# Kernel tuning notes

Hardware: AMD Instinct MI355X
Metric: run time of the kernel (lower is better)

Reference implementation:

```python
import jax, jax.numpy as jnp
import numpy as np

B, N, DIM, HID = 32, 10000, 64, 128


def _linear_params(key, fan_in, fan_out):
    kw, kb = jax.random.split(key)
    bound = 1.0 / np.sqrt(fan_in)
    w = jax.random.uniform(kw, (fan_out, fan_in), jnp.float32, -bound, bound)
    b = jax.random.uniform(kb, (fan_out,), jnp.float32, -bound, bound)
    return w, b


def setup_inputs() -> dict:
    key = jax.random.key(0)
    ks = jax.random.split(key, 7)
    x = jax.random.normal(ks[0], (B, N, DIM), jnp.float32)
    adj_col = jax.random.uniform(ks[1], (N,), jnp.float32)
    n2e_w, n2e_b = _linear_params(ks[2], 2 * DIM, HID)
    e2e_w, e2e_b = _linear_params(ks[3], HID, HID)
    e2n_w, e2n_b = _linear_params(ks[4], HID, HID)
    n2n_w, n2n_b = _linear_params(ks[5], HID, HID)
    out_w, out_b = _linear_params(ks[6], DIM + HID, DIM)
    return {
        "x": x, "adj_col": adj_col,
        "n2e_w": n2e_w, "n2e_b": n2e_b,
        "e2e_w": e2e_w, "e2e_b": e2e_b,
        "e2n_w": e2n_w, "e2n_b": e2n_b,
        "n2n_w": n2n_w, "n2n_b": n2n_b,
        "out_w": out_w, "out_b": out_b,
        "i": 5, "num": 4, "node_size": 2000,
    }


def reference(x, adj_col, n2e_w, n2e_b, e2e_w, e2e_b, e2n_w, e2n_b,
              n2n_w, n2n_b, out_w, out_b, i, num, node_size):
    # The torch loop over (num+1) chunks is an execution tiling; mathematically it
    # computes a full sum over all N nodes. We vectorize it in one pass.
    starter = x[:, i, :]                                   # [B, dim]
    ender = jnp.broadcast_to(starter[:, None, :], x.shape)  # [B, N, dim]
    c = jnp.concatenate([x, ender], axis=-1)               # [B, N, 2*dim]
    h = jax.nn.relu(jnp.einsum('bnd,hd->bnh', c, n2e_w) + n2e_b)
    h = jax.nn.relu(jnp.einsum('bnh,gh->bng', h, e2e_w) + e2e_b)
    h = h * adj_col[None, :, None]                         # adjacency mask
    s = jnp.sum(h, axis=1)                                 # [B, hid]
    y = jax.nn.relu(s @ e2n_w.T + e2n_b)
    y = jax.nn.relu(y @ n2n_w.T + n2n_b)
    out = jnp.concatenate([starter, y], axis=-1) @ out_w.T + out_b  # [B, dim]
    return out
```

## Files before the change

### kernel.cpp

```cpp
#include <hip/hip_runtime.h>
#include <hip/hip_bf16.h>

typedef float f32x4 __attribute__((ext_vector_type(4)));
typedef short bf16x8 __attribute__((ext_vector_type(8)));
typedef unsigned short u16;
typedef unsigned int u32;

#define NB 32
#define NN 10000
#define DIMX 64

__device__ __forceinline__ u16 f2bf(float f) {
    union { float f; unsigned u; } v; v.f = f;
    unsigned r = (v.u + 0x7FFFu + ((v.u >> 16) & 1u)) >> 16;
    return (u16)r;
}

__device__ __forceinline__ u32 pkbf(float a, float b) {
    __hip_bfloat162 h = __float22bfloat162_rn(make_float2(a, b));
    u32 r; __builtin_memcpy(&r, &h, 4); return r;
}

__global__ void k_prep(const float* __restrict__ x, const float* __restrict__ n2e_w,
                       const float* __restrict__ n2e_b, const float* __restrict__ e2e_w,
                       const int* __restrict__ ip,
                       float* __restrict__ bias1, u16* __restrict__ w1p, u16* __restrict__ w2p) {
    int id = blockIdx.x * 256 + threadIdx.x;
    if (id < 4096) {
        int b = id >> 7, j = id & 127;
        int i = ip[0];
        const float* xr = x + ((size_t)b * NN + i) * DIMX;
        const float* w = n2e_w + j * 128 + 64;
        float s = n2e_b[j];
        #pragma unroll
        for (int d = 0; d < 64; ++d) s += xr[d] * w[d];
        bias1[b * 128 + j] = s;
    } else if (id < 12288) {
        int e = id - 4096;
        int i8 = e & 7, lane = (e >> 3) & 63, kk = (e >> 9) & 1, t = e >> 10;
        int row = t * 16 + (lane & 15), col = kk * 32 + (lane >> 4) * 8 + i8;
        w1p[e] = f2bf(n2e_w[row * 128 + col]);
    } else if (id < 28672) {
        int e = id - 12288;
        int i8 = e & 7, lane = (e >> 3) & 63, kk = (e >> 9) & 3, t = e >> 11;
        int row = t * 16 + (lane & 15), col = kk * 32 + (lane >> 4) * 8 + i8;
        w2p[e] = f2bf(e2e_w[row * 128 + col]);
    }
}

__global__ __launch_bounds__(256, 2) void k_main(
        const float* __restrict__ x, const float* __restrict__ adj,
        const float* __restrict__ bias1, const u16* __restrict__ w1p,
        const u16* __restrict__ w2p, const float* __restrict__ e2e_b,
        float* __restrict__ partials) {
    __shared__ u16 sW1[8192];
    __shared__ u16 sW2[16384];
    __shared__ u16 sH1[8192];
    __shared__ float sBias[128];

    const int tid = threadIdx.x;
    const int lane = tid & 63, wave = tid >> 6;
    const int c = lane & 15, g = lane >> 4;
    const int pair = wave >> 1, wh = wave & 1;
    const int bid = blockIdx.x;
    const int b = bid >> 4, qb = bid & 15;
    const int s0 = qb ? qb * 39 + 1 : 0;
    const int cnt = qb ? 39 : 40;

    #pragma unroll
    for (int p = 0; p < 4; ++p) { int o = (p * 256 + tid) * 8;
        *(bf16x8*)&sW1[o] = *(const bf16x8*)&w1p[o]; }
    #pragma unroll
    for (int p = 0; p < 8; ++p) { int o = (p * 256 + tid) * 8;
        *(bf16x8*)&sW2[o] = *(const bf16x8*)&w2p[o]; }
    if (tid < 128) sBias[tid] = bias1[b * 128 + tid];

    float b2v[4];
    #pragma unroll
    for (int tt = 0; tt < 4; ++tt) b2v[tt] = e2e_b[(wh * 4 + tt) * 16 + c];

    float sAcc[4] = {0.f,0.f,0.f,0.f};
    __syncthreads();

    const size_t xbatch = (size_t)b * NN;
    u16* const pairH = &sH1[pair * 4096];

    for (int it = 0; it < 5; ++it) {
        const int base_idx = it * 8 + pair * 4;

        bf16x8 A1[2][2];
        #pragma unroll
        for (int s = 0; s < 2; ++s) {
            int idx = base_idx + wh * 2 + s;
            int stl = idx < cnt ? idx : cnt - 1;
            int row0 = (s0 + stl) * 16;
            const float* xr = x + (xbatch + row0 + c) * 64 + g * 8;
            #pragma unroll
            for (int kk = 0; kk < 2; ++kk) {
                f32x4 lo = *(const f32x4*)(xr + kk * 32);
                f32x4 hi = *(const f32x4*)(xr + kk * 32 + 4);
                union { bf16x8 v; u32 w[4]; } u;
                u.w[0] = pkbf(lo[0], lo[1]); u.w[1] = pkbf(lo[2], lo[3]);
                u.w[2] = pkbf(hi[0], hi[1]); u.w[3] = pkbf(hi[2], hi[3]);
                A1[s][kk] = u.v;
            }
        }
        f32x4 adjv[4];
        #pragma unroll
        for (int sub = 0; sub < 4; ++sub) {
            int idx = base_idx + sub;
            if (idx < cnt) adjv[sub] = *(const f32x4*)(adj + (s0 + idx) * 16 + 4 * g);
            else adjv[sub] = (f32x4){0.f,0.f,0.f,0.f};
        }

        f32x4 acc[4][4];
        #pragma unroll
        for (int sub = 0; sub < 4; ++sub)
            #pragma unroll
            for (int tt = 0; tt < 4; ++tt) acc[sub][tt] = (f32x4){0.f,0.f,0.f,0.f};

        #pragma unroll
        for (int kk2 = 0; kk2 < 4; ++kk2) {
            u16* const bufH = pairH + (kk2 & 1) * 2048;
            const int t0 = kk2 * 2, t1 = kk2 * 2 + 1;
            bf16x8 w1a0 = *(const bf16x8*)&sW1[(t0 * 2 + 0) * 512 + lane * 8];
            bf16x8 w1b0 = *(const bf16x8*)&sW1[(t0 * 2 + 1) * 512 + lane * 8];
            bf16x8 w1a1 = *(const bf16x8*)&sW1[(t1 * 2 + 0) * 512 + lane * 8];
            bf16x8 w1b1 = *(const bf16x8*)&sW1[(t1 * 2 + 1) * 512 + lane * 8];
            f32x4 cb0 = *(const f32x4*)&sBias[t0 * 16 + 4 * g];
            f32x4 cb1 = *(const f32x4*)&sBias[t1 * 16 + 4 * g];
            #pragma unroll
            for (int s = 0; s < 2; ++s) {
                f32x4 d0 = __builtin_amdgcn_mfma_f32_16x16x32_bf16(w1a0, A1[s][0], cb0, 0, 0, 0);
                d0 = __builtin_amdgcn_mfma_f32_16x16x32_bf16(w1b0, A1[s][1], d0, 0, 0, 0);
                f32x4 d1 = __builtin_amdgcn_mfma_f32_16x16x32_bf16(w1a1, A1[s][0], cb1, 0, 0, 0);
                d1 = __builtin_amdgcn_mfma_f32_16x16x32_bf16(w1b1, A1[s][1], d1, 0, 0, 0);
                u32 p00 = pkbf(fmaxf(d0[0], 0.f), fmaxf(d0[1], 0.f));
                u32 p01 = pkbf(fmaxf(d0[2], 0.f), fmaxf(d0[3], 0.f));
                u32 p10 = pkbf(fmaxf(d1[0], 0.f), fmaxf(d1[1], 0.f));
                u32 p11 = pkbf(fmaxf(d1[2], 0.f), fmaxf(d1[3], 0.f));
                int slice = (wh * 2 + s) * 512;
                int base = c * 64;
                int swz = 16 * (c & 3);
                *(uint2*)&bufH[slice + ((base + ((8 * g) ^ swz)) >> 1)]      = make_uint2(p00, p01);
                *(uint2*)&bufH[slice + ((base + ((32 + 8 * g) ^ swz)) >> 1)] = make_uint2(p10, p11);
            }
            __syncthreads();
            bf16x8 A2[4];
            #pragma unroll
            for (int sub = 0; sub < 4; ++sub)
                A2[sub] = *(const bf16x8*)&bufH[sub * 512 + ((c * 64 + 16 * (g ^ (c & 3))) >> 1)];
            #pragma unroll
            for (int tt = 0; tt < 4; ++tt) {
                const int t2 = wh * 4 + tt;
                bf16x8 w2f = *(const bf16x8*)&sW2[(t2 * 4 + kk2) * 512 + lane * 8];
                #pragma unroll
                for (int sub = 0; sub < 4; ++sub)
                    acc[sub][tt] = __builtin_amdgcn_mfma_f32_16x16x32_bf16(A2[sub], w2f, acc[sub][tt], 0, 0, 0);
            }
        }

        #pragma unroll
        for (int tt = 0; tt < 4; ++tt) {
            float bb = b2v[tt];
            #pragma unroll
            for (int sub = 0; sub < 4; ++sub)
                #pragma unroll
                for (int r = 0; r < 4; ++r)
                    sAcc[tt] = fmaf(adjv[sub][r], fmaxf(acc[sub][tt][r] + bb, 0.f), sAcc[tt]);
        }
    }

    #pragma unroll
    for (int tt = 0; tt < 4; ++tt) {
        float v = sAcc[tt];
        v += __shfl_xor(v, 16, 64);
        v += __shfl_xor(v, 32, 64);
        sAcc[tt] = v;
    }
    __syncthreads();
    float* sRed = (float*)sW1;
    if (lane < 16) {
        #pragma unroll
        for (int tt = 0; tt < 4; ++tt) sRed[wave * 64 + tt * 16 + lane] = sAcc[tt];
    }
    __syncthreads();
    if (tid < 128) {
        int t2 = tid >> 4, jc = tid & 15;
        int tt = t2 & 3, w0 = t2 >> 2;
        partials[bid * 128 + tid] =
            sRed[w0 * 64 + tt * 16 + jc] + sRed[(w0 + 2) * 64 + tt * 16 + jc];
    }
}

__global__ void k_final(const float* __restrict__ partials, const float* __restrict__ x,
                        const int* __restrict__ ip,
                        const float* __restrict__ e2n_w, const float* __restrict__ e2n_b,
                        const float* __restrict__ n2n_w, const float* __restrict__ n2n_b,
                        const float* __restrict__ out_w, const float* __restrict__ out_b,
                        float* __restrict__ out) {
    int b = blockIdx.x, j = threadIdx.x;
    __shared__ float s0[128], s1[128], s2[128];
    float acc = 0.f;
    #pragma unroll
    for (int qq = 0; qq < 16; ++qq) acc += partials[(b * 16 + qq) * 128 + j];
    s0[j] = acc;
    __syncthreads();
    {
        float a1 = e2n_b[j];
        const float* w = e2n_w + j * 128;
        #pragma unroll 8
        for (int k = 0; k < 128; ++k) a1 += w[k] * s0[k];
        s1[j] = fmaxf(a1, 0.f);
    }
    __syncthreads();
    {
        float a2 = n2n_b[j];
        const float* w = n2n_w + j * 128;
        #pragma unroll 8
        for (int k = 0; k < 128; ++k) a2 += w[k] * s1[k];
        s2[j] = fmaxf(a2, 0.f);
    }
    __syncthreads();
    if (j < 64) {
        int i = ip[0];
        const float* xr = x + ((size_t)b * NN + i) * DIMX;
        const float* ow = out_w + j * 192;
        float o = out_b[j];
        #pragma unroll 8
        for (int m = 0; m < 64; ++m) o += ow[m] * xr[m];
        #pragma unroll 8
        for (int m = 0; m < 128; ++m) o += ow[64 + m] * s2[m];
        out[b * 64 + j] = o;
    }
}

extern "C" void kernel_launch(void* const* d_in, const int* in_sizes, int n_in,
                              void* d_out, int out_size, void* d_ws, size_t ws_size,
                              hipStream_t stream) {
    const float* x      = (const float*)d_in[0];
    const float* adj    = (const float*)d_in[1];
    const float* n2e_w  = (const float*)d_in[2];
    const float* n2e_b  = (const float*)d_in[3];
    const float* e2e_w  = (const float*)d_in[4];
    const float* e2e_b  = (const float*)d_in[5];
    const float* e2n_w  = (const float*)d_in[6];
    const float* e2n_b  = (const float*)d_in[7];
    const float* n2n_w  = (const float*)d_in[8];
    const float* n2n_b  = (const float*)d_in[9];
    const float* out_w  = (const float*)d_in[10];
    const float* out_b  = (const float*)d_in[11];
    const int*   ip     = (const int*)d_in[12];
    float* out = (float*)d_out;

    char* ws = (char*)d_ws;
    float* bias1    = (float*)ws;
    u16*   w1p      = (u16*)(ws + 16384);
    u16*   w2p      = (u16*)(ws + 32768);
    float* partials = (float*)(ws + 65536);

    k_prep<<<112, 256, 0, stream>>>(x, n2e_w, n2e_b, e2e_w, ip, bias1, w1p, w2p);
    k_main<<<512, 256, 0, stream>>>(x, adj, bias1, w1p, w2p, e2e_b, partials);
    k_final<<<32, 128, 0, stream>>>(partials, x, ip, e2n_w, e2n_b, n2n_w, n2n_b,
                                    out_w, out_b, out);
}
```

Baseline: 51.87 us.

## Keep W2 fragments in registers, prefetch x, double-buffer H1, raise occupancy

The main kernel stops staging the second-layer weight matrix in shared memory. Each wave now holds its own 32 output columns of W2 in registers, which frees LDS for a double-buffered H1 tile. The block count rises from 512 to 768 (24 chunks per batch) and the launch bound allows 3 blocks per CU. Each wave processes one 16-row sub-tile per iteration with a register prefetch of the next x rows, and needs a single barrier per iteration instead of four. The block-level reduction is dropped because each wave writes its partial sums directly. The trade-offs are higher register pressure, since W2 fragments stay live for the whole kernel, and more partials for the final kernel to sum.

```diff
diff --git a/kernel.cpp b/kernel.cpp
--- a/kernel.cpp
+++ b/kernel.cpp
@@ -48,80 +48,80 @@
     }
 }
 
-__global__ __launch_bounds__(256, 2) void k_main(
+__global__ __launch_bounds__(256, 3) void k_main(
         const float* __restrict__ x, const float* __restrict__ adj,
         const float* __restrict__ bias1, const u16* __restrict__ w1p,
         const u16* __restrict__ w2p, const float* __restrict__ e2e_b,
         float* __restrict__ partials) {
     __shared__ u16 sW1[8192];
-    __shared__ u16 sW2[16384];
-    __shared__ u16 sH1[8192];
-    __shared__ float sBias[128];
+    __shared__ u16 sH1[16384];
+    __shared__ float sBias[256];
 
     const int tid = threadIdx.x;
     const int lane = tid & 63, wave = tid >> 6;
     const int c = lane & 15, g = lane >> 4;
-    const int pair = wave >> 1, wh = wave & 1;
     const int bid = blockIdx.x;
-    const int b = bid >> 4, qb = bid & 15;
-    const int s0 = qb ? qb * 39 + 1 : 0;
-    const int cnt = qb ? 39 : 40;
+    const int b = bid / 24, qb = bid - b * 24;
+    const int s0 = qb ? 27 + (qb - 1) * 26 : 0;
+    const int cnt = qb ? 26 : 27;
 
     #pragma unroll
     for (int p = 0; p < 4; ++p) { int o = (p * 256 + tid) * 8;
         *(bf16x8*)&sW1[o] = *(const bf16x8*)&w1p[o]; }
-    #pragma unroll
-    for (int p = 0; p < 8; ++p) { int o = (p * 256 + tid) * 8;
-        *(bf16x8*)&sW2[o] = *(const bf16x8*)&w2p[o]; }
     if (tid < 128) sBias[tid] = bias1[b * 128 + tid];
-
-    float b2v[4];
-    #pragma unroll
-    for (int tt = 0; tt < 4; ++tt) b2v[tt] = e2e_b[(wh * 4 + tt) * 16 + c];
-
-    float sAcc[4] = {0.f,0.f,0.f,0.f};
+    else if (tid < 256) sBias[tid] = e2e_b[tid - 128];
+
+    const bf16x8* const gW2 = (const bf16x8*)w2p;
+    bf16x8 w2r[2][4];
+    #pragma unroll
+    for (int tt = 0; tt < 2; ++tt)
+        #pragma unroll
+        for (int kk2 = 0; kk2 < 4; ++kk2)
+            w2r[tt][kk2] = gW2[((wave * 2 + tt) * 4 + kk2) * 64 + lane];
+
+    float sAcc[2] = {0.f, 0.f};
     __syncthreads();
 
     const size_t xbatch = (size_t)b * NN;
-    u16* const pairH = &sH1[pair * 4096];
-
-    for (int it = 0; it < 5; ++it) {
-        const int base_idx = it * 8 + pair * 4;
-
-        bf16x8 A1[2][2];
-        #pragma unroll
-        for (int s = 0; s < 2; ++s) {
-            int idx = base_idx + wh * 2 + s;
+    const int swzW = 16 * (c & 3);
+    const int rdOff = (c * 64 + 16 * (g ^ (c & 3))) >> 1;
+
+    f32x4 xl[4];
+    {
+        int idx = wave;
+        int stl = idx < cnt ? idx : cnt - 1;
+        const float* xr = x + (xbatch + (s0 + stl) * 16 + c) * 64 + g * 8;
+        xl[0] = *(const f32x4*)(xr);
+        xl[1] = *(const f32x4*)(xr + 4);
+        xl[2] = *(const f32x4*)(xr + 32);
+        xl[3] = *(const f32x4*)(xr + 36);
+    }
+
+    int par = 0;
+    #pragma unroll 1
+    for (int it = 0; it < 7; ++it) {
+        bf16x8 A1[2];
+        #pragma unroll
+        for (int kk = 0; kk < 2; ++kk) {
+            f32x4 lo = xl[kk * 2], hi = xl[kk * 2 + 1];
+            union { bf16x8 v; u32 w[4]; } u;
+            u.w[0] = pkbf(lo[0], lo[1]); u.w[1] = pkbf(lo[2], lo[3]);
+            u.w[2] = pkbf(hi[0], hi[1]); u.w[3] = pkbf(hi[2], hi[3]);
+            A1[kk] = u.v;
+        }
+        if (it < 6) {
+            int idx = (it + 1) * 4 + wave;
             int stl = idx < cnt ? idx : cnt - 1;
-            int row0 = (s0 + stl) * 16;
-            const float* xr = x + (xbatch + row0 + c) * 64 + g * 8;
-            #pragma unroll
-            for (int kk = 0; kk < 2; ++kk) {
-                f32x4 lo = *(const f32x4*)(xr + kk * 32);
-                f32x4 hi = *(const f32x4*)(xr + kk * 32 + 4);
-                union { bf16x8 v; u32 w[4]; } u;
-                u.w[0] = pkbf(lo[0], lo[1]); u.w[1] = pkbf(lo[2], lo[3]);
-                u.w[2] = pkbf(hi[0], hi[1]); u.w[3] = pkbf(hi[2], hi[3]);
-                A1[s][kk] = u.v;
-            }
-        }
-        f32x4 adjv[4];
-        #pragma unroll
-        for (int sub = 0; sub < 4; ++sub) {
-            int idx = base_idx + sub;
-            if (idx < cnt) adjv[sub] = *(const f32x4*)(adj + (s0 + idx) * 16 + 4 * g);
-            else adjv[sub] = (f32x4){0.f,0.f,0.f,0.f};
-        }
-
-        f32x4 acc[4][4];
-        #pragma unroll
-        for (int sub = 0; sub < 4; ++sub)
-            #pragma unroll
-            for (int tt = 0; tt < 4; ++tt) acc[sub][tt] = (f32x4){0.f,0.f,0.f,0.f};
-
+            const float* xr = x + (xbatch + (s0 + stl) * 16 + c) * 64 + g * 8;
+            xl[0] = *(const f32x4*)(xr);
+            xl[1] = *(const f32x4*)(xr + 4);
+            xl[2] = *(const f32x4*)(xr + 32);
+            xl[3] = *(const f32x4*)(xr + 36);
+        }
+
+        u16* const bufW = &sH1[par * 8192 + wave * 512];
         #pragma unroll
         for (int kk2 = 0; kk2 < 4; ++kk2) {
-            u16* const bufH = pairH + (kk2 & 1) * 2048;
             const int t0 = kk2 * 2, t1 = kk2 * 2 + 1;
             bf16x8 w1a0 = *(const bf16x8*)&sW1[(t0 * 2 + 0) * 512 + lane * 8];
             bf16x8 w1b0 = *(const bf16x8*)&sW1[(t0 * 2 + 1) * 512 + lane * 8];
@@ -129,67 +129,70 @@
             bf16x8 w1b1 = *(const bf16x8*)&sW1[(t1 * 2 + 1) * 512 + lane * 8];
             f32x4 cb0 = *(const f32x4*)&sBias[t0 * 16 + 4 * g];
             f32x4 cb1 = *(const f32x4*)&sBias[t1 * 16 + 4 * g];
-            #pragma unroll
-            for (int s = 0; s < 2; ++s) {
-                f32x4 d0 = __builtin_amdgcn_mfma_f32_16x16x32_bf16(w1a0, A1[s][0], cb0, 0, 0, 0);
-                d0 = __builtin_amdgcn_mfma_f32_16x16x32_bf16(w1b0, A1[s][1], d0, 0, 0, 0);
-                f32x4 d1 = __builtin_amdgcn_mfma_f32_16x16x32_bf16(w1a1, A1[s][0], cb1, 0, 0, 0);
-                d1 = __builtin_amdgcn_mfma_f32_16x16x32_bf16(w1b1, A1[s][1], d1, 0, 0, 0);
-                u32 p00 = pkbf(fmaxf(d0[0], 0.f), fmaxf(d0[1], 0.f));
-                u32 p01 = pkbf(fmaxf(d0[2], 0.f), fmaxf(d0[3], 0.f));
-                u32 p10 = pkbf(fmaxf(d1[0], 0.f), fmaxf(d1[1], 0.f));
-                u32 p11 = pkbf(fmaxf(d1[2], 0.f), fmaxf(d1[3], 0.f));
-                int slice = (wh * 2 + s) * 512;
-                int base = c * 64;
-                int swz = 16 * (c & 3);
-                *(uint2*)&bufH[slice + ((base + ((8 * g) ^ swz)) >> 1)]      = make_uint2(p00, p01);
-                *(uint2*)&bufH[slice + ((base + ((32 + 8 * g) ^ swz)) >> 1)] = make_uint2(p10, p11);
-            }
-            __syncthreads();
+            f32x4 d0 = __builtin_amdgcn_mfma_f32_16x16x32_bf16(w1a0, A1[0], cb0, 0, 0, 0);
+            d0 = __builtin_amdgcn_mfma_f32_16x16x32_bf16(w1b0, A1[1], d0, 0, 0, 0);
+            f32x4 d1 = __builtin_amdgcn_mfma_f32_16x16x32_bf16(w1a1, A1[0], cb1, 0, 0, 0);
+            d1 = __builtin_amdgcn_mfma_f32_16x16x32_bf16(w1b1, A1[1], d1, 0, 0, 0);
+            u32 p00 = pkbf(fmaxf(d0[0], 0.f), fmaxf(d0[1], 0.f));
+            u32 p01 = pkbf(fmaxf(d0[2], 0.f), fmaxf(d0[3], 0.f));
+            u32 p10 = pkbf(fmaxf(d1[0], 0.f), fmaxf(d1[1], 0.f));
+            u32 p11 = pkbf(fmaxf(d1[2], 0.f), fmaxf(d1[3], 0.f));
+            int base = c * 64;
+            *(uint2*)&bufW[kk2 * 2048 + ((base + ((8 * g) ^ swzW)) >> 1)]      = make_uint2(p00, p01);
+            *(uint2*)&bufW[kk2 * 2048 + ((base + ((32 + 8 * g) ^ swzW)) >> 1)] = make_uint2(p10, p11);
+        }
+        __syncthreads();
+
+        f32x4 acc[4][2];
+        #pragma unroll
+        for (int sub = 0; sub < 4; ++sub)
+            #pragma unroll
+            for (int tt = 0; tt < 2; ++tt) acc[sub][tt] = (f32x4){0.f,0.f,0.f,0.f};
+        const u16* const bufR = &sH1[par * 8192];
+        #pragma unroll
+        for (int kk2 = 0; kk2 < 4; ++kk2) {
             bf16x8 A2[4];
             #pragma unroll
             for (int sub = 0; sub < 4; ++sub)
-                A2[sub] = *(const bf16x8*)&bufH[sub * 512 + ((c * 64 + 16 * (g ^ (c & 3))) >> 1)];
-            #pragma unroll
-            for (int tt = 0; tt < 4; ++tt) {
-                const int t2 = wh * 4 + tt;
-                bf16x8 w2f = *(const bf16x8*)&sW2[(t2 * 4 + kk2) * 512 + lane * 8];
+                A2[sub] = *(const bf16x8*)&bufR[kk2 * 2048 + sub * 512 + rdOff];
+            #pragma unroll
+            for (int tt = 0; tt < 2; ++tt)
                 #pragma unroll
                 for (int sub = 0; sub < 4; ++sub)
-                    acc[sub][tt] = __builtin_amdgcn_mfma_f32_16x16x32_bf16(A2[sub], w2f, acc[sub][tt], 0, 0, 0);
-            }
-        }
-
-        #pragma unroll
-        for (int tt = 0; tt < 4; ++tt) {
-            float bb = b2v[tt];
+                    acc[sub][tt] = __builtin_amdgcn_mfma_f32_16x16x32_bf16(A2[sub], w2r[tt][kk2], acc[sub][tt], 0, 0, 0);
+        }
+
+        f32x4 adjv[4];
+        #pragma unroll
+        for (int sub = 0; sub < 4; ++sub) {
+            int idx = it * 4 + sub;
+            if (idx < cnt) adjv[sub] = *(const f32x4*)(adj + (s0 + idx) * 16 + 4 * g);
+            else adjv[sub] = (f32x4){0.f,0.f,0.f,0.f};
+        }
+        #pragma unroll
+        for (int tt = 0; tt < 2; ++tt) {
+            float bb = sBias[128 + (wave * 2 + tt) * 16 + c];
             #pragma unroll
             for (int sub = 0; sub < 4; ++sub)
                 #pragma unroll
                 for (int r = 0; r < 4; ++r)
                     sAcc[tt] = fmaf(adjv[sub][r], fmaxf(acc[sub][tt][r] + bb, 0.f), sAcc[tt]);
         }
-    }
-
-    #pragma unroll
-    for (int tt = 0; tt < 4; ++tt) {
+        par ^= 1;
+    }
+
+    float red[2];
+    #pragma unroll
+    for (int tt = 0; tt < 2; ++tt) {
         float v = sAcc[tt];
         v += __shfl_xor(v, 16, 64);
         v += __shfl_xor(v, 32, 64);
-        sAcc[tt] = v;
-    }
-    __syncthreads();
-    float* sRed = (float*)sW1;
+        red[tt] = v;
+    }
     if (lane < 16) {
         #pragma unroll
-        for (int tt = 0; tt < 4; ++tt) sRed[wave * 64 + tt * 16 + lane] = sAcc[tt];
-    }
-    __syncthreads();
-    if (tid < 128) {
-        int t2 = tid >> 4, jc = tid & 15;
-        int tt = t2 & 3, w0 = t2 >> 2;
-        partials[bid * 128 + tid] =
-            sRed[w0 * 64 + tt * 16 + jc] + sRed[(w0 + 2) * 64 + tt * 16 + jc];
+        for (int tt = 0; tt < 2; ++tt)
+            partials[bid * 128 + (wave * 2 + tt) * 16 + lane] = red[tt];
     }
 }
 
@@ -203,7 +206,7 @@
     __shared__ float s0[128], s1[128], s2[128];
     float acc = 0.f;
     #pragma unroll
-    for (int qq = 0; qq < 16; ++qq) acc += partials[(b * 16 + qq) * 128 + j];
+    for (int qq = 0; qq < 24; ++qq) acc += partials[(b * 24 + qq) * 128 + j];
     s0[j] = acc;
     __syncthreads();
     {
@@ -260,7 +263,7 @@
     float* partials = (float*)(ws + 65536);
 
     k_prep<<<112, 256, 0, stream>>>(x, n2e_w, n2e_b, e2e_w, ip, bias1, w1p, w2p);
-    k_main<<<512, 256, 0, stream>>>(x, adj, bias1, w1p, w2p, e2e_b, partials);
+    k_main<<<768, 256, 0, stream>>>(x, adj, bias1, w1p, w2p, e2e_b, partials);
     k_final<<<32, 128, 0, stream>>>(partials, x, ip, e2n_w, e2n_b, n2n_w, n2n_b,
                                     out_w, out_b, out);
 }
```

After: 46.99 us. 1.1x faster.
